# Kernel optimization log

Measured on AMD Instinct MI355X. Metric: run time of the kernel, lower is better.

## Reference

```python
import math
import jax, jax.numpy as jnp
import numpy as np

DYNAMIC_TOP = 8
PATCH_EQUIV = 16
EPS = 1e-8  # torch cosine_similarity eps


def setup_inputs() -> dict:
    key = jax.random.key(0)
    k1, k2 = jax.random.split(key)
    x = jax.random.normal(k1, (64, 785, 768), dtype=jnp.float32)
    images = jax.random.normal(k2, (64, 3, 448, 448), dtype=jnp.float32)
    return {"x": x, "images": images}


def _crop_resize(img, x0, x1, y0, y1, out_size):
    """Bilinear resize (align_corners=True, matching F.upsample_bilinear) of the
    dynamic crop img[:, x0:x1, y0:y1] to (out_size, out_size), via gathers."""
    t = jnp.arange(out_size, dtype=jnp.float32)
    h = (x1 - x0).astype(jnp.float32)
    w = (y1 - y0).astype(jnp.float32)
    scale = 1.0 / (out_size - 1)
    sy = x0.astype(jnp.float32) + t * (h - 1.0) * scale  # source rows
    sx = y0.astype(jnp.float32) + t * (w - 1.0) * scale  # source cols
    y_lo = jnp.floor(sy).astype(jnp.int32)
    x_lo = jnp.floor(sx).astype(jnp.int32)
    y_hi = jnp.minimum(y_lo + 1, x1 - 1)
    x_hi = jnp.minimum(x_lo + 1, y1 - 1)
    wy = (sy - y_lo.astype(jnp.float32))[:, None]  # [out, 1]
    wx = (sx - x_lo.astype(jnp.float32))[None, :]  # [1, out]

    def gat(yi, xi):  # -> [C, out, out]
        return img[:, yi[:, None], xi[None, :]]

    return ((1.0 - wy) * (1.0 - wx) * gat(y_lo, x_lo)
            + (1.0 - wy) * wx * gat(y_lo, x_hi)
            + wy * (1.0 - wx) * gat(y_hi, x_lo)
            + wy * wx * gat(y_hi, x_hi))


def reference(x, images):
    img_size = images.shape[-1]
    g = x[:, :1, :]   # [B, 1, D] cls token (global)
    l = x[:, 1:, :]   # [B, S, D] local tokens

    # cosine similarity (torch eps semantics: clamp each norm at eps)
    gn = jnp.maximum(jnp.linalg.norm(g, axis=-1), EPS)  # [B, 1]
    ln = jnp.maximum(jnp.linalg.norm(l, axis=-1), EPS)  # [B, S]
    distances = jnp.sum(g * l, axis=-1) / (gn * ln)      # [B, S]

    top, ind = jax.lax.top_k(distances, DYNAMIC_TOP)     # largest=True

    fh = int(math.sqrt(x.shape[1]))  # uses full seq len incl. cls, as in source
    ind_x = (ind // fh).astype(jnp.int32)
    ind_y = (ind % fh).astype(jnp.int32)
    x_i = jnp.min(ind_x, axis=-1) * PATCH_EQUIV
    x_f = jnp.max(ind_x, axis=-1) * PATCH_EQUIV
    y_i = jnp.min(ind_y, axis=-1) * PATCH_EQUIV
    y_f = jnp.max(ind_y, axis=-1) * PATCH_EQUIV

    x0 = jnp.maximum(x_i, 0)
    y0 = jnp.maximum(y_i, 0)
    x1 = jnp.minimum(jnp.maximum(x_f, x_i + PATCH_EQUIV), img_size)
    y1 = jnp.minimum(jnp.maximum(y_f, y_i + PATCH_EQUIV), img_size)

    crops = jax.vmap(lambda im, a, b, c, d: _crop_resize(im, a, b, c, d, img_size))(
        images, x0, x1, y0, y1)  # [B, C, img_size, img_size]
    return crops
```

## Files before the change

kernel.cpp:

```cpp
#include <hip/hip_runtime.h>
#include <math.h>

#define BATCH 64
#define TOK   784
#define DIM   768
#define FH    28
#define IMG   448
#define TOPK  8
#define PE    16

__global__ __launch_bounds__(256) void dist_kernel(const float* __restrict__ x,
                                                   float* __restrict__ dist) {
    const int b    = blockIdx.y;
    const int wave = threadIdx.x >> 6;
    const int lane = threadIdx.x & 63;
    const int t    = blockIdx.x * 4 + wave;

    const float4* g = (const float4*)(x + (size_t)b * 785 * DIM);
    const float4* l = (const float4*)(x + (size_t)b * 785 * DIM + (size_t)(1 + t) * DIM);

    float dot = 0.f, l2 = 0.f, g2 = 0.f;
#pragma unroll
    for (int k = 0; k < 3; ++k) {
        float4 gv = g[lane + 64 * k];
        float4 lv = l[lane + 64 * k];
        dot += gv.x * lv.x + gv.y * lv.y + gv.z * lv.z + gv.w * lv.w;
        l2  += lv.x * lv.x + lv.y * lv.y + lv.z * lv.z + lv.w * lv.w;
        g2  += gv.x * gv.x + gv.y * gv.y + gv.z * gv.z + gv.w * gv.w;
    }
#pragma unroll
    for (int off = 32; off > 0; off >>= 1) {
        dot += __shfl_xor(dot, off);
        l2  += __shfl_xor(l2, off);
        g2  += __shfl_xor(g2, off);
    }
    if (lane == 0) {
        float gn = fmaxf(sqrtf(g2), 1e-8f);
        float ln = fmaxf(sqrtf(l2), 1e-8f);
        dist[b * TOK + t] = dot / (gn * ln);
    }
}

__global__ __launch_bounds__(256) void topk_kernel(const float* __restrict__ dist,
                                                   int4* __restrict__ boxes) {
    const int b   = blockIdx.x;
    const int tid = threadIdx.x;
    __shared__ float sd[TOK];
    __shared__ float rv[256];
    __shared__ int   ri[256];
    __shared__ int sel_minx, sel_maxx, sel_miny, sel_maxy;

    for (int i = tid; i < TOK; i += 256) sd[i] = dist[b * TOK + i];
    if (tid == 0) { sel_minx = 1 << 30; sel_maxx = -1; sel_miny = 1 << 30; sel_maxy = -1; }
    __syncthreads();

    for (int iter = 0; iter < TOPK; ++iter) {
        float best = -INFINITY;
        int   bi   = TOK;
        for (int i = tid; i < TOK; i += 256) {
            float v = sd[i];
            if (v > best || (v == best && i < bi)) { best = v; bi = i; }
        }
        rv[tid] = best;
        ri[tid] = bi;
        __syncthreads();
        for (int s = 128; s > 0; s >>= 1) {
            if (tid < s) {
                float v2 = rv[tid + s];
                int   i2 = ri[tid + s];
                if (v2 > rv[tid] || (v2 == rv[tid] && i2 < ri[tid])) {
                    rv[tid] = v2;
                    ri[tid] = i2;
                }
            }
            __syncthreads();
        }
        if (tid == 0) {
            int idx = ri[0];
            sd[idx] = -INFINITY;
            int ix = idx / FH, iy = idx % FH;
            sel_minx = min(sel_minx, ix); sel_maxx = max(sel_maxx, ix);
            sel_miny = min(sel_miny, iy); sel_maxy = max(sel_maxy, iy);
        }
        __syncthreads();
    }

    if (tid == 0) {
        int x_i = sel_minx * PE, x_f = sel_maxx * PE;
        int y_i = sel_miny * PE, y_f = sel_maxy * PE;
        int x0 = max(x_i, 0);
        int y0 = max(y_i, 0);
        int x1 = min(max(x_f, x_i + PE), IMG);
        int y1 = min(max(y_f, y_i + PE), IMG);
        boxes[b] = make_int4(x0, x1, y0, y1);
    }
}

__global__ __launch_bounds__(256) void resize_kernel(const float* __restrict__ images,
                                                     const int4* __restrict__ boxes,
                                                     float* __restrict__ out) {
    const int b = blockIdx.z;
    const int c = blockIdx.y;
    const int pix = (blockIdx.x * 256 + threadIdx.x) * 4;
    const int i = pix / IMG;
    const int j = pix % IMG;

    const int4 box = boxes[b];
    const float x0 = (float)box.x;
    const int   x1 = box.y;
    const float y0 = (float)box.z;
    const int   y1 = box.w;
    const float h = (float)(x1 - box.x);
    const float w = (float)(y1 - box.z);
    const float scale = 1.0f / (float)(IMG - 1);

    float sy = x0 + ((float)i * (h - 1.0f)) * scale;
    int   y_lo = (int)floorf(sy);
    int   y_hi = min(y_lo + 1, x1 - 1);
    float wy   = sy - (float)y_lo;

    const float* img = images + ((size_t)b * 3 + c) * (IMG * IMG);
    const float* rlo = img + y_lo * IMG;
    const float* rhi = img + y_hi * IMG;

    float res[4];
#pragma unroll
    for (int k = 0; k < 4; ++k) {
        float sx = y0 + ((float)(j + k) * (w - 1.0f)) * scale;
        int   x_lo = (int)floorf(sx);
        int   x_hi = min(x_lo + 1, y1 - 1);
        float wx   = sx - (float)x_lo;
        float a  = rlo[x_lo];
        float bb = rlo[x_hi];
        float cc = rhi[x_lo];
        float dd = rhi[x_hi];
        res[k] = (1.f - wy) * ((1.f - wx) * a + wx * bb) +
                 wy * ((1.f - wx) * cc + wx * dd);
    }
    float4 o = make_float4(res[0], res[1], res[2], res[3]);
    *(float4*)(out + ((size_t)b * 3 + c) * (IMG * IMG) + pix) = o;
}

extern "C" void kernel_launch(void* const* d_in, const int* in_sizes, int n_in,
                              void* d_out, int out_size, void* d_ws, size_t ws_size,
                              hipStream_t stream) {
    const float* x      = (const float*)d_in[0];
    const float* images = (const float*)d_in[1];
    float*       out    = (float*)d_out;

    float* dist  = (float*)d_ws;
    int4*  boxes = (int4*)((char*)d_ws + BATCH * TOK * sizeof(float));

    dist_kernel<<<dim3(TOK / 4, BATCH), 256, 0, stream>>>(x, dist);
    topk_kernel<<<BATCH, 256, 0, stream>>>(dist, boxes);
    resize_kernel<<<dim3(IMG * IMG / 1024, 3, BATCH), 256, 0, stream>>>(images, boxes, out);
}
```

Before: 420.7 us.

## Stage source rows in LDS for resize and use single-wave register top-k

Top-k is rewritten as a single wavefront that keeps its 13 distance values per lane in registers and reduces with shuffles, removing the shared-memory tree reduction and block barriers. The resize kernel now gives each block four output rows, loads the needed source rows (at most five) into LDS with coalesced float4 loads, and then gathers from LDS, writing scalar coalesced stores. This aims to replace scattered global gathers with staged shared-memory reads. It adds a barrier and drops the vectorised output store. Clamping to five rows assumes the crop height never magnifies rows beyond that range, which holds for this crop scheme.

After: 355.1 us. -15.6%, faster.

```diff
diff --git a/kernel.cpp b/kernel.cpp
--- a/kernel.cpp
+++ b/kernel.cpp
@@ -41,53 +41,43 @@
     }
 }
 
-__global__ __launch_bounds__(256) void topk_kernel(const float* __restrict__ dist,
-                                                   int4* __restrict__ boxes) {
-    const int b   = blockIdx.x;
-    const int tid = threadIdx.x;
-    __shared__ float sd[TOK];
-    __shared__ float rv[256];
-    __shared__ int   ri[256];
-    __shared__ int sel_minx, sel_maxx, sel_miny, sel_maxy;
+__global__ __launch_bounds__(64) void topk_kernel(const float* __restrict__ dist,
+                                                  int4* __restrict__ boxes) {
+    const int b    = blockIdx.x;
+    const int lane = threadIdx.x;
 
-    for (int i = tid; i < TOK; i += 256) sd[i] = dist[b * TOK + i];
-    if (tid == 0) { sel_minx = 1 << 30; sel_maxx = -1; sel_miny = 1 << 30; sel_maxy = -1; }
-    __syncthreads();
+    float v[13];
+#pragma unroll
+    for (int k = 0; k < 13; ++k) {
+        int t = lane + 64 * k;
+        v[k] = (t < TOK) ? dist[b * TOK + t] : -INFINITY;
+    }
+
+    int minx = 1 << 30, maxx = -1, miny = 1 << 30, maxy = -1;
 
     for (int iter = 0; iter < TOPK; ++iter) {
         float best = -INFINITY;
-        int   bi   = TOK;
-        for (int i = tid; i < TOK; i += 256) {
-            float v = sd[i];
-            if (v > best || (v == best && i < bi)) { best = v; bi = i; }
+        int   bk   = 0;
+#pragma unroll
+        for (int k = 0; k < 13; ++k) {
+            if (v[k] > best) { best = v[k]; bk = k; }
         }
-        rv[tid] = best;
-        ri[tid] = bi;
-        __syncthreads();
-        for (int s = 128; s > 0; s >>= 1) {
-            if (tid < s) {
-                float v2 = rv[tid + s];
-                int   i2 = ri[tid + s];
-                if (v2 > rv[tid] || (v2 == rv[tid] && i2 < ri[tid])) {
-                    rv[tid] = v2;
-                    ri[tid] = i2;
-                }
-            }
-            __syncthreads();
+        int bidx = lane + 64 * bk;
+#pragma unroll
+        for (int off = 32; off > 0; off >>= 1) {
+            float ov = __shfl_xor(best, off);
+            int   oi = __shfl_xor(bidx, off);
+            if (ov > best || (ov == best && oi < bidx)) { best = ov; bidx = oi; }
         }
-        if (tid == 0) {
-            int idx = ri[0];
-            sd[idx] = -INFINITY;
-            int ix = idx / FH, iy = idx % FH;
-            sel_minx = min(sel_minx, ix); sel_maxx = max(sel_maxx, ix);
-            sel_miny = min(sel_miny, iy); sel_maxy = max(sel_maxy, iy);
-        }
-        __syncthreads();
+        if ((bidx & 63) == lane) v[bidx >> 6] = -INFINITY;
+        int ix = bidx / FH, iy = bidx % FH;
+        minx = min(minx, ix); maxx = max(maxx, ix);
+        miny = min(miny, iy); maxy = max(maxy, iy);
     }
 
-    if (tid == 0) {
-        int x_i = sel_minx * PE, x_f = sel_maxx * PE;
-        int y_i = sel_miny * PE, y_f = sel_maxy * PE;
+    if (lane == 0) {
+        int x_i = minx * PE, x_f = maxx * PE;
+        int y_i = miny * PE, y_f = maxy * PE;
         int x0 = max(x_i, 0);
         int y0 = max(y_i, 0);
         int x1 = min(max(x_f, x_i + PE), IMG);
@@ -99,34 +89,55 @@
 __global__ __launch_bounds__(256) void resize_kernel(const float* __restrict__ images,
                                                      const int4* __restrict__ boxes,
                                                      float* __restrict__ out) {
-    const int b = blockIdx.z;
-    const int c = blockIdx.y;
-    const int pix = (blockIdx.x * 256 + threadIdx.x) * 4;
-    const int i = pix / IMG;
-    const int j = pix % IMG;
+    const int b    = blockIdx.z;
+    const int c    = blockIdx.y;
+    const int r0   = blockIdx.x * 4;
+    const int tid  = threadIdx.x;
+    const int lane = tid & 63;
+    const int rblk = tid >> 6;
 
     const int4 box = boxes[b];
-    const float x0 = (float)box.x;
-    const int   x1 = box.y;
-    const float y0 = (float)box.z;
-    const int   y1 = box.w;
+    const float x0f = (float)box.x;
+    const int   x1  = box.y;
+    const float y0f = (float)box.z;
+    const int   y1  = box.w;
     const float h = (float)(x1 - box.x);
     const float w = (float)(y1 - box.z);
     const float scale = 1.0f / (float)(IMG - 1);
 
-    float sy = x0 + ((float)i * (h - 1.0f)) * scale;
+    const float sy0 = x0f + (float)r0 * (h - 1.0f) * scale;
+    const float sy3 = x0f + (float)(r0 + 3) * (h - 1.0f) * scale;
+    const int rbase = (int)floorf(sy0);
+    int rlast = min((int)floorf(sy3) + 1, x1 - 1);
+    int nrows = rlast - rbase + 1;
+    nrows = max(1, min(nrows, 5));
+
+    __shared__ float srows[5][IMG];
+
+    const float* img = images + ((size_t)b * 3 + c) * (IMG * IMG);
+    const int total = nrows * (IMG / 4);
+    for (int i = tid; i < total; i += 256) {
+        int r  = i / (IMG / 4);
+        int c4 = i - r * (IMG / 4);
+        float4 vv = *(const float4*)(img + (size_t)(rbase + r) * IMG + c4 * 4);
+        *(float4*)&srows[r][c4 * 4] = vv;
+    }
+    __syncthreads();
+
+    const int row = r0 + rblk;
+    const float sy = x0f + (float)row * (h - 1.0f) * scale;
     int   y_lo = (int)floorf(sy);
     int   y_hi = min(y_lo + 1, x1 - 1);
     float wy   = sy - (float)y_lo;
 
-    const float* img = images + ((size_t)b * 3 + c) * (IMG * IMG);
-    const float* rlo = img + y_lo * IMG;
-    const float* rhi = img + y_hi * IMG;
+    const float* rlo = srows[y_lo - rbase];
+    const float* rhi = srows[y_hi - rbase];
+    float* orow = out + (((size_t)b * 3 + c) * IMG + row) * IMG;
 
-    float res[4];
 #pragma unroll
-    for (int k = 0; k < 4; ++k) {
-        float sx = y0 + ((float)(j + k) * (w - 1.0f)) * scale;
+    for (int kk = 0; kk < 7; ++kk) {
+        int j = lane + 64 * kk;
+        float sx = y0f + (float)j * (w - 1.0f) * scale;
         int   x_lo = (int)floorf(sx);
         int   x_hi = min(x_lo + 1, y1 - 1);
         float wx   = sx - (float)x_lo;
@@ -134,11 +145,9 @@
         float bb = rlo[x_hi];
         float cc = rhi[x_lo];
         float dd = rhi[x_hi];
-        res[k] = (1.f - wy) * ((1.f - wx) * a + wx * bb) +
-                 wy * ((1.f - wx) * cc + wx * dd);
+        orow[j] = (1.f - wy) * ((1.f - wx) * a + wx * bb) +
+                  wy * ((1.f - wx) * cc + wx * dd);
     }
-    float4 o = make_float4(res[0], res[1], res[2], res[3]);
-    *(float4*)(out + ((size_t)b * 3 + c) * (IMG * IMG) + pix) = o;
 }
 
 extern "C" void kernel_launch(void* const* d_in, const int* in_sizes, int n_in,
@@ -152,6 +161,6 @@
     int4*  boxes = (int4*)((char*)d_ws + BATCH * TOK * sizeof(float));
 
     dist_kernel<<<dim3(TOK / 4, BATCH), 256, 0, stream>>>(x, dist);
-    topk_kernel<<<BATCH, 256, 0, stream>>>(dist, boxes);
-    resize_kernel<<<dim3(IMG * IMG / 1024, 3, BATCH), 256, 0, stream>>>(images, boxes, out);
+    topk_kernel<<<BATCH, 64, 0, stream>>>(dist, boxes);
+    resize_kernel<<<dim3(IMG / 4, 3, BATCH), 256, 0, stream>>>(images, boxes, out);
 }
```
